# Kernel optimization log

Measured on AMD Instinct MI355X. Metric: run time of the kernel, lower is better.

## Reference

```python
import jax, jax.numpy as jnp
import numpy as np

B, HH, WW, E = 8, 64, 64, 384
NH, EXP = 6, 2
D1 = (EXP * E) // NH * NH      # 768
HD = D1 // NH                  # 128
RPE = 512
LAYERS = 3
EPS = 1e-6


def srms(x):
    # SimpleRMSNorm: no learnable weight
    return x * jax.lax.rsqrt(jnp.mean(x * x, axis=-1, keepdims=True) + EPS)


def rpe_forward(pos, pw, pb, lw, lb, ow, ob):
    # pos: (n, 1) -> (n, NH*HD). Rpe MLP: act(pos_proj) -> layers x [norm,act,linear] -> out
    x = jax.nn.relu(pos @ pw + pb)
    for i in range(lw.shape[0]):  # fixed small layer count
        x = jax.nn.relu(srms(x)) @ lw[i] + lb[i]
    return jax.nn.relu(srms(x)) @ ow + ob


def tno_coeffs(n, pw, pb, lw, lb, ow, ob):
    # Toeplitz coeffs t_0..t_{n-1}, t_0(dummy), t_{-(n-1)}..t_{-1} for circular conv of len 2n
    pos = jnp.arange(1, n, dtype=jnp.float32)[:, None]             # (n-1, 1), par_type=1
    neg = -jnp.arange(1, n, dtype=jnp.float32)[::-1][:, None]      # -(n-1)..-1
    zero = jnp.zeros((1, 1), dtype=jnp.float32)
    t_zero = rpe_forward(zero, pw, pb, lw, lb, ow, ob)             # (1, NH*HD)
    t_pos = rpe_forward(pos, pw, pb, lw, lb, ow, ob)               # (n-1, NH*HD)
    t_neg = rpe_forward(neg, pw, pb, lw, lb, ow, ob)
    a = jnp.concatenate([t_zero, t_pos, t_zero, t_neg], axis=0)    # (2n, NH*HD)
    return a.reshape(2 * n, NH, HD).transpose(1, 0, 2)             # (NH, 2n, HD)


def tno_apply(v, a, axis):
    # v: (b, h, H, W, d); FFT-based Toeplitz (circular) mixing along `axis` in {-3, -2}
    n = v.shape[axis]
    a = a[:, :, None, :] if axis == -3 else a[:, None, :, :]
    y = jnp.fft.rfft(v, 2 * n, axis=axis)
    af = jnp.fft.rfft(a, 2 * n, axis=axis)
    out = jnp.fft.irfft(af * y, 2 * n, axis=axis)
    return jax.lax.slice_in_dim(out, 0, n, axis=out.ndim + axis)


def setup_inputs() -> dict:
    key = jax.random.key(0)
    ks = jax.random.split(key, 24)
    s = 0.02
    def rn(k, shape):
        return jax.random.normal(k, shape, dtype=jnp.float32) * s
    inp = {
        "x": jax.random.normal(ks[0], (B, HH, WW, E), dtype=jnp.float32),
        "H": HH, "W": WW,
        "Wu": rn(ks[1], (E, D1)), "bu": jnp.zeros((D1,), jnp.float32),
        "Wv": rn(ks[2], (E, D1)), "bv": jnp.zeros((D1,), jnp.float32),
        "Wo": rn(ks[3], (D1, E)), "bo": jnp.zeros((E,), jnp.float32),
    }
    for t, off in (("r1", 4), ("r2", 10)):
        inp[t + "_pw"] = rn(ks[off], (1, RPE))
        inp[t + "_pb"] = jnp.zeros((RPE,), jnp.float32)
        inp[t + "_lw"] = rn(ks[off + 1], (LAYERS, RPE, RPE))
        inp[t + "_lb"] = jnp.zeros((LAYERS, RPE), jnp.float32)
        inp[t + "_ow"] = rn(ks[off + 2], (RPE, NH * HD))
        inp[t + "_ob"] = jnp.zeros((NH * HD,), jnp.float32)
    return inp


def reference(x, H, W, Wu, bu, Wv, bv, Wo, bo,
              r1_pw, r1_pb, r1_lw, r1_lb, r1_ow, r1_ob,
              r2_pw, r2_pb, r2_lw, r2_lb, r2_ow, r2_ob):
    b = x.shape[0]
    xn = srms(x)                                    # pre_norm (SimpleRMSNorm)
    u = jax.nn.silu(xn @ Wu + bu)                   # gate branch
    v = jax.nn.silu(xn @ Wv + bv)
    v = v.reshape(b, H, W, NH, HD).transpose(0, 3, 1, 2, 4)        # b h H W d
    a_h = tno_coeffs(H, r2_pw, r2_pb, r2_lw, r2_lb, r2_ow, r2_ob)  # toep2, dim=-3
    a_w = tno_coeffs(W, r1_pw, r1_pb, r1_lw, r1_lb, r1_ow, r1_ob)  # toep1, dim=-2
    out = tno_apply(v, a_h, -3) + tno_apply(v, a_w, -2)
    out = out.transpose(0, 2, 3, 1, 4).reshape(b, H, W, NH * HD)   # b H W (h d)
    out = u * out
    return out @ Wo + bo + x
```

## Files before the change

kernel.cpp:

```cpp
#include <hip/hip_runtime.h>
#include <stdint.h>


typedef __attribute__((ext_vector_type(4))) float  f32x4;
typedef __attribute__((ext_vector_type(8))) short  s16x8;
typedef __attribute__((ext_vector_type(8))) unsigned short u16x8;
typedef __attribute__((ext_vector_type(4))) unsigned short u16x4;
typedef unsigned short u16;

#define M_TOT 32768

__device__ __forceinline__ u16 f2bf(float f) {
  union { float f; unsigned int u; } v; v.f = f;
  unsigned int r = (v.u + 0x7FFFu + ((v.u >> 16) & 1u)) >> 16;
  return (u16)r;
}
__device__ __forceinline__ float bf2f(u16 h) {
  union { unsigned int u; float f; } v; v.u = ((unsigned int)h) << 16;
  return v.f;
}
__device__ __forceinline__ float silu_f(float x) {
  return x * __builtin_amdgcn_rcpf(1.f + __expf(-x));
}

__device__ __forceinline__ void gload_lds16(const u16* g, u16* l) {
  __builtin_amdgcn_global_load_lds(
      (const __attribute__((address_space(1))) uint32_t*)g,
      (__attribute__((address_space(3))) uint32_t*)l, 16, 0, 0);
}

__global__ __launch_bounds__(256) void setup_k(
    const float* __restrict__ x, u16* __restrict__ xn,
    const float* __restrict__ Wu, const float* __restrict__ Wv,
    const float* __restrict__ Wo, u16* __restrict__ Wuvt, u16* __restrict__ Wot,
    const float* __restrict__ r1lw, const float* __restrict__ r1ow,
    const float* __restrict__ r2lw, const float* __restrict__ r2ow,
    u16* __restrict__ lwT, u16* __restrict__ owT,
    const float* __restrict__ r1pw, const float* __restrict__ r1pb,
    const float* __restrict__ r2pw, const float* __restrict__ r2pb,
    float* __restrict__ X0) {
  __shared__ float sm[32][33];
  const int bid = blockIdx.x;
  const int tid = threadIdx.x;

  if (bid < 8192) {
    int row  = bid * 4 + (tid >> 6);
    int lane = tid & 63;
    const float* xr = x + (size_t)row * 384 + lane;
    float v[6]; float ss = 0.f;
#pragma unroll
    for (int i = 0; i < 6; i++) { v[i] = xr[i * 64]; ss += v[i] * v[i]; }
#pragma unroll
    for (int off = 32; off > 0; off >>= 1) ss += __shfl_xor(ss, off);
    float sc = rsqrtf(ss * (1.f / 384.f) + 1e-6f);
    u16* o = xn + (size_t)row * 384 + lane;
#pragma unroll
    for (int i = 0; i < 6; i++) o[i * 64] = f2bf(v[i] * sc);
  } else if (bid < 11360) {
    int b = bid - 8192;
    const float* src; u16* dst; int C, DS, R0, C0;
    if (b < 2304) {
      int mlp = b / 1152, r = b % 1152;
      if (r < 768) {
        int L = r / 256, t = r % 256;
        R0 = (t / 16) * 32; C0 = (t % 16) * 32;
        src = (mlp ? r2lw : r1lw) + (size_t)L * 262144;
        dst = lwT + (size_t)(mlp * 3 + L) * 262144;
        C = 512; DS = 512;
      } else {
        int t = r - 768;
        R0 = (t / 24) * 32; C0 = (t % 24) * 32;
        src = mlp ? r2ow : r1ow;
        dst = owT + (size_t)mlp * 393216;
        C = 768; DS = 512;
      }
    } else {
      int t = b - 2304;
      if (t < 288)      { R0 = (t / 24) * 32; C0 = (t % 24) * 32;
                          src = Wu; C = 768; dst = Wuvt;             DS = 384; }
      else if (t < 576) { int t2 = t - 288; R0 = (t2 / 24) * 32; C0 = (t2 % 24) * 32;
                          src = Wv; C = 768; dst = Wuvt + 768 * 384; DS = 384; }
      else              { int t2 = t - 576; R0 = (t2 / 12) * 32; C0 = (t2 % 12) * 32;
                          src = Wo; C = 384; dst = Wot;              DS = 768; }
    }
    int lx = tid % 32, ly = tid / 32;
#pragma unroll
    for (int q = 0; q < 4; q++) {
      int y = q * 8 + ly;
      sm[y][lx] = src[(size_t)(R0 + y) * C + C0 + lx];
    }
    __syncthreads();
#pragma unroll
    for (int q = 0; q < 4; q++) {
      int y = q * 8 + ly;
      dst[(size_t)(C0 + y) * DS + R0 + lx] = f2bf(sm[lx][y]);
    }
  } else {
    int idx = (bid - 11360) * 256 + tid;
    int gid = idx * 4;
    int row = gid >> 9, col = gid & 511;
    int mlp = row >> 7, p = row & 127;
    float pos = (p < 64) ? (float)p : ((p == 64) ? 0.f : (float)(p - 128));
    const float* pw = (mlp ? r2pw : r1pw) + col;
    const float* pb = (mlp ? r2pb : r1pb) + col;
    f32x4 w = *(const f32x4*)pw;
    f32x4 bb = *(const f32x4*)pb;
    f32x4 o;
#pragma unroll
    for (int e = 0; e < 4; e++) o[e] = fmaxf(pos * w[e] + bb[e], 0.f);
    *(f32x4*)(X0 + gid) = o;
  }
}

template <int N, bool TOUT>
__global__ __launch_bounds__(256) void rpe_layer_k(
    const float* __restrict__ X,
    const u16* __restrict__ wtA, const u16* __restrict__ wtB,
    const float* __restrict__ bA, const float* __restrict__ bB,
    float* __restrict__ outA, float* __restrict__ outB) {
  constexpr int NSL = N / 64;
  const int mlp = blockIdx.x / NSL;
  const int n0  = (blockIdx.x % NSL) * 64;
  const u16* WT = mlp ? wtB : wtA;
  const float* bias = mlp ? bB : bA;
  float* out = mlp ? outB : outA;
  const float* Xm = X + (size_t)mlp * 128 * 512;

  __shared__ __align__(16) u16 Bs[64 * 512];
  __shared__ __align__(16) u16 As[2][128 * 64];
  __shared__ float scale[128];

  const int tid  = threadIdx.x;
  const int lane = tid & 63;
  const int w    = tid >> 6;
  const int fl   = lane & 15, fh = lane >> 4;

#pragma unroll
  for (int r = 0; r < 16; r++) {
    int row  = r * 4 + w;
    int csrc = (lane & ~7) | ((lane & 7) ^ (row & 7));
    gload_lds16(WT + (size_t)(n0 + row) * 512 + csrc * 8,
                Bs + row * 512 + lane * 8);
  }

  {
    int row = tid >> 1, half = tid & 1;
    const float* xr = Xm + (size_t)row * 512 + half * 256;
    float ss = 0.f;
#pragma unroll 8
    for (int q = 0; q < 64; q++) {
      f32x4 v = *(const f32x4*)(xr + q * 4);
      ss += v[0] * v[0] + v[1] * v[1] + v[2] * v[2] + v[3] * v[3];
    }
    ss += __shfl_xor(ss, 1);
    if (!half) scale[row] = rsqrtf(ss * (1.f / 512.f) + 1e-6f);
  }
  __syncthreads();

  int arow[4], akc[4];
  float s_[4];
#pragma unroll
  for (int q = 0; q < 4; q++) {
    int cid = q * 256 + tid;
    arow[q] = cid >> 3;
    akc[q]  = cid & 7;
    s_[q]   = scale[arow[q]];
  }

#pragma unroll
  for (int q = 0; q < 4; q++) {
    const float* xp = Xm + (size_t)arow[q] * 512 + akc[q] * 8;
    f32x4 v0 = *(const f32x4*)xp;
    f32x4 v1 = *(const f32x4*)(xp + 4);
    u16x8 pk;
#pragma unroll
    for (int e = 0; e < 4; e++) pk[e]     = f2bf(fmaxf(v0[e], 0.f) * s_[q]);
#pragma unroll
    for (int e = 0; e < 4; e++) pk[4 + e] = f2bf(fmaxf(v1[e], 0.f) * s_[q]);
    *(u16x8*)(&As[0][arow[q] * 64 + ((akc[q] ^ (arow[q] & 7)) * 8)]) = pk;
  }
  __syncthreads();

  f32x4 acc[2][4];
  {
    f32x4 z = {0.f, 0.f, 0.f, 0.f};
#pragma unroll
    for (int i = 0; i < 2; i++)
#pragma unroll
      for (int j = 0; j < 4; j++) acc[i][j] = z;
  }

  for (int kti = 0; kti < 8; kti++) {
    const int cur = kti & 1;
    f32x4 pf0[4], pf1[4];
    if (kti < 7) {
#pragma unroll
      for (int q = 0; q < 4; q++) {
        const float* xp = Xm + (size_t)arow[q] * 512 + (kti + 1) * 64 + akc[q] * 8;
        pf0[q] = *(const f32x4*)xp;
        pf1[q] = *(const f32x4*)(xp + 4);
      }
    }
#pragma unroll
    for (int ks = 0; ks < 2; ks++) {
      const int xc = ((ks * 4 + fh) ^ (fl & 7)) * 8;
      s16x8 af[2], bfr[4];
#pragma unroll
      for (int i = 0; i < 2; i++)
        af[i] = *(const s16x8*)(&As[cur][(w * 32 + i * 16 + fl) * 64 + xc]);
#pragma unroll
      for (int j = 0; j < 4; j++)
        bfr[j] = *(const s16x8*)(&Bs[(j * 16 + fl) * 512 + kti * 64 + xc]);
#pragma unroll
      for (int i = 0; i < 2; i++)
#pragma unroll
        for (int j = 0; j < 4; j++)
          acc[i][j] = __builtin_amdgcn_mfma_f32_16x16x32_bf16(af[i], bfr[j], acc[i][j], 0, 0, 0);
    }
    if (kti < 7) {
#pragma unroll
      for (int q = 0; q < 4; q++) {
        u16x8 pk;
#pragma unroll
        for (int e = 0; e < 4; e++) pk[e]     = f2bf(fmaxf(pf0[q][e], 0.f) * s_[q]);
#pragma unroll
        for (int e = 0; e < 4; e++) pk[4 + e] = f2bf(fmaxf(pf1[q][e], 0.f) * s_[q]);
        *(u16x8*)(&As[cur ^ 1][arow[q] * 64 + ((akc[q] ^ (arow[q] & 7)) * 8)]) = pk;
      }
    }
    __syncthreads();
  }

#pragma unroll
  for (int i = 0; i < 2; i++)
#pragma unroll
    for (int j = 0; j < 4; j++) {
      int c = n0 + j * 16 + fl;
      float bv_ = bias[c];
#pragma unroll
      for (int q = 0; q < 4; q++) {
        int r = w * 32 + i * 16 + fh * 4 + q;
        if (TOUT) out[(size_t)c * 128 + r] = acc[i][j][q] + bv_;
        else      out[(size_t)r * N + c]   = acc[i][j][q] + bv_;
      }
    }
}

__global__ __launch_bounds__(256) void gemm0_k(
    const u16* __restrict__ A, const u16* __restrict__ Bt,
    u16* __restrict__ u_out, u16* __restrict__ vt_out,
    const float* __restrict__ bu, const float* __restrict__ bv) {
  __shared__ __align__(16) char smem[34816];
  u16*   As  = (u16*)smem;
  u16*   Bs  = As + 128 * 64;
  float* epi = (float*)smem;

  const int tid  = threadIdx.x;
  const int lane = tid & 63;
  const int wid  = tid >> 6;
  const int wm   = wid >> 1, wn = wid & 1;
  const int bm   = blockIdx.x & 255, bn = blockIdx.x >> 8;
  const int m0   = bm * 128, n0 = bn * 128;
  const int fl   = lane & 15, fh = lane >> 4;
  const int K    = 384;

  f32x4 acc[4][4];
  {
    f32x4 z = {0.f, 0.f, 0.f, 0.f};
#pragma unroll
    for (int i = 0; i < 4; i++)
#pragma unroll
      for (int j = 0; j < 4; j++) acc[i][j] = z;
  }

  const int sr  = tid >> 3;
  const int scl = (tid & 7) * 8;
  const int scs = ((tid & 7) ^ (sr & 7)) * 8;

  for (int kt = 0; kt < K; kt += 64) {
    const u16* gA = A  + (size_t)(m0 + sr) * K + kt + scs;
    const u16* gB = Bt + (size_t)(n0 + sr) * K + kt + scs;
    u16* lA = As + sr * 64 + scl;
    u16* lB = Bs + sr * 64 + scl;
#pragma unroll
    for (int i = 0; i < 4; i++) {
      gload_lds16(gA + (size_t)(i * 32) * K, lA + i * 32 * 64);
      gload_lds16(gB + (size_t)(i * 32) * K, lB + i * 32 * 64);
    }
    __syncthreads();
#pragma unroll
    for (int ks = 0; ks < 2; ks++) {
      s16x8 af[4], bfr[4];
      const int xc = ((ks * 4 + fh) ^ (fl & 7)) * 8;
      const u16* ap = As + (wm * 64 + fl) * 64 + xc;
      const u16* bp = Bs + (wn * 64 + fl) * 64 + xc;
#pragma unroll
      for (int i = 0; i < 4; i++) af[i] = *(const s16x8*)(ap + i * 16 * 64);
#pragma unroll
      for (int j = 0; j < 4; j++) bfr[j] = *(const s16x8*)(bp + j * 16 * 64);
#pragma unroll
      for (int i = 0; i < 4; i++)
#pragma unroll
        for (int j = 0; j < 4; j++)
          acc[i][j] = __builtin_amdgcn_mfma_f32_16x16x32_bf16(af[i], bfr[j], acc[i][j], 0, 0, 0);
    }
    __syncthreads();
  }

  for (int half = 0; half < 2; half++) {
    __syncthreads();
    if (wm == half) {
#pragma unroll
      for (int i = 0; i < 4; i++)
#pragma unroll
        for (int j = 0; j < 4; j++) {
          int er = i * 16 + fh * 4;
          int ec = wn * 64 + j * 16 + fl;
#pragma unroll
          for (int q = 0; q < 4; q++) epi[(er + q) * 132 + ec] = acc[i][j][q];
        }
    }
    __syncthreads();
    const bool isU = (n0 < 768);
    u16* baseo = isU ? u_out : vt_out;
    const int cc = tid >> 1;
    const int cg = (isU ? n0 : n0 - 768) + cc;
    const float bias_v = (isU ? bu : bv)[cg];
    u16* dst = baseo + (size_t)cg * M_TOT + m0 + half * 64;
#pragma unroll
    for (int q = 0; q < 4; q++) {
      int mb = (tid & 1) * 8 + q * 16;
      u16x8 pk;
#pragma unroll
      for (int e = 0; e < 8; e++) {
        int mm = mb + e;
        pk[e] = f2bf(silu_f(epi[mm * 132 + cc] + bias_v));
      }
      *(u16x8*)(dst + mb) = pk;
    }
  }
}

__global__ __launch_bounds__(512, 2) void gemm2_k(
    const u16* __restrict__ gT, const u16* __restrict__ Wot,
    float* __restrict__ out, const float* __restrict__ bo,
    const float* __restrict__ xres) {
  __shared__ __align__(16) u16 As[128 * 64];
  __shared__ __align__(16) u16 Bs[384 * 64];

  const int tid  = threadIdx.x;
  const int lane = tid & 63;
  const int wid  = tid >> 6;
  const int wm   = wid >> 2;
  const int wn   = wid & 3;
  const int m0   = blockIdx.x * 128;
  const int fl   = lane & 15, fh = lane >> 4;

  f32x4 acc[4][6];
  {
    f32x4 z = {0.f, 0.f, 0.f, 0.f};
#pragma unroll
    for (int i = 0; i < 4; i++)
#pragma unroll
      for (int j = 0; j < 6; j++) acc[i][j] = z;
  }

  const int sr  = tid >> 3;
  const int scl = (tid & 7) * 8;
  const int scs = ((tid & 7) ^ (sr & 7)) * 8;

  for (int kt = 0; kt < 768; kt += 64) {
#pragma unroll
    for (int i = 0; i < 6; i++)
      gload_lds16(Wot + (size_t)(sr + 64 * i) * 768 + kt + scs,
                  Bs + (sr + 64 * i) * 64 + scl);
#pragma unroll
    for (int r = 0; r < 2; r++) {
      int cid = r * 512 + tid;
      int row = cid >> 4;
      int cm  = cid & 15;
      const u16* ga = gT + (size_t)(kt + row) * M_TOT + m0 + cm * 8;
      u16x8 rv = *(const u16x8*)ga;
      int kc = row >> 3, of = row & 7;
#pragma unroll
      for (int e = 0; e < 8; e++)
        As[(cm * 8 + e) * 64 + ((kc ^ e) << 3) + of] = rv[e];
    }
    __syncthreads();
#pragma unroll
    for (int ks = 0; ks < 2; ks++) {
      s16x8 af[4], bfr[6];
      const int xc = ((ks * 4 + fh) ^ (fl & 7)) * 8;
      const u16* ap = As + (wm * 64 + fl) * 64 + xc;
      const u16* bp = Bs + (wn * 96 + fl) * 64 + xc;
#pragma unroll
      for (int i = 0; i < 4; i++) af[i] = *(const s16x8*)(ap + i * 16 * 64);
#pragma unroll
      for (int j = 0; j < 6; j++) bfr[j] = *(const s16x8*)(bp + j * 16 * 64);
#pragma unroll
      for (int i = 0; i < 4; i++)
#pragma unroll
        for (int j = 0; j < 6; j++)
          acc[i][j] = __builtin_amdgcn_mfma_f32_16x16x32_bf16(af[i], bfr[j], acc[i][j], 0, 0, 0);
    }
    __syncthreads();
  }

  float bov[6];
#pragma unroll
  for (int j = 0; j < 6; j++) bov[j] = bo[wn * 96 + j * 16 + fl];
#pragma unroll
  for (int i = 0; i < 4; i++) {
#pragma unroll
    for (int q = 0; q < 4; q++) {
      int m = m0 + wm * 64 + i * 16 + fh * 4 + q;
      const float* xr = xres + (size_t)m * 384;
      float* orow = out + (size_t)m * 384;
#pragma unroll
      for (int j = 0; j < 6; j++) {
        int n = wn * 96 + j * 16 + fl;
        orow[n] = acc[i][j][q] + bov[j] + xr[n];
      }
    }
  }
}

__global__ __launch_bounds__(256) void conv_k(const u16* __restrict__ vt,
                                              const u16* __restrict__ ut,
                                              const float* __restrict__ a_hT,
                                              const float* __restrict__ a_wT,
                                              u16* __restrict__ gT) {
  __shared__ __align__(16) u16 Th[64 * 72];
  __shared__ __align__(16) u16 Tw[64 * 72];
  __shared__ __align__(16) u16 Vs[64 * 72];
  __shared__ __align__(16) u16 VTs[64 * 72];
  __shared__ __align__(16) u16 Us[64 * 72];
  __shared__ float ahr[192];
  __shared__ float awr[192];
  u16* epi = VTs;

  const int tid = threadIdx.x;
  const int c = blockIdx.x;
  const int lane = tid & 63, w = tid >> 6;
  const int fl = lane & 15, fh = lane >> 4;

  if (tid < 192) {
    int idx = (128 - tid) & 127;
    ahr[tid] = a_hT[(size_t)c * 128 + idx];
    awr[tid] = a_wT[(size_t)c * 128 + idx];
  }
  __syncthreads();

  {
    int y = tid & 63, j0 = (tid >> 6) * 16;
    int base = 128 - y + j0;
    u16x8 p0, p1, q0, q1;
#pragma unroll
    for (int e = 0; e < 8; e++) {
      p0[e] = f2bf(ahr[base + e]);
      p1[e] = f2bf(ahr[base + 8 + e]);
      q0[e] = f2bf(awr[base + e]);
      q1[e] = f2bf(awr[base + 8 + e]);
    }
    *(u16x8*)(Th + y * 72 + j0)     = p0;
    *(u16x8*)(Th + y * 72 + j0 + 8) = p1;
    *(u16x8*)(Tw + y * 72 + j0)     = q0;
    *(u16x8*)(Tw + y * 72 + j0 + 8) = q1;
  }

  const int sy = tid >> 2, sx = (tid & 3) * 16;
  const int ty = tid & 63, tj = (tid >> 6) * 16;

  for (int b = 0; b < 8; b++) {
    const u16* srcv = vt + (size_t)c * M_TOT + b * 4096;
    const u16* srcu = ut + (size_t)c * M_TOT + b * 4096;
    *(u16x8*)(Vs + sy * 72 + sx)     = *(const u16x8*)(srcv + sy * 64 + sx);
    *(u16x8*)(Vs + sy * 72 + sx + 8) = *(const u16x8*)(srcv + sy * 64 + sx + 8);
    *(u16x8*)(Us + sy * 72 + sx)     = *(const u16x8*)(srcu + sy * 64 + sx);
    *(u16x8*)(Us + sy * 72 + sx + 8) = *(const u16x8*)(srcu + sy * 64 + sx + 8);
    __syncthreads();

    {
      u16x8 q0 = *(const u16x8*)(Vs + ty * 72 + tj);
      u16x8 q1 = *(const u16x8*)(Vs + ty * 72 + tj + 8);
#pragma unroll
      for (int e = 0; e < 8; e++) VTs[(tj + e) * 72 + ty]     = q0[e];
#pragma unroll
      for (int e = 0; e < 8; e++) VTs[(tj + 8 + e) * 72 + ty] = q1[e];
    }
    __syncthreads();

    f32x4 acc[4];
    {
      f32x4 z = {0.f, 0.f, 0.f, 0.f};
#pragma unroll
      for (int i = 0; i < 4; i++) acc[i] = z;
    }
#pragma unroll
    for (int ks = 0; ks < 2; ks++) {
      s16x8 qh = *(const s16x8*)(Th + (w * 16 + fl) * 72 + ks * 32 + fh * 8);
#pragma unroll
      for (int i = 0; i < 4; i++) {
        s16x8 p = *(const s16x8*)(VTs + (i * 16 + fl) * 72 + ks * 32 + fh * 8);
        acc[i] = __builtin_amdgcn_mfma_f32_16x16x32_bf16(p, qh, acc[i], 0, 0, 0);
      }
      s16x8 qw = *(const s16x8*)(Vs + (w * 16 + fl) * 72 + ks * 32 + fh * 8);
#pragma unroll
      for (int i = 0; i < 4; i++) {
        s16x8 p = *(const s16x8*)(Tw + (i * 16 + fl) * 72 + ks * 32 + fh * 8);
        acc[i] = __builtin_amdgcn_mfma_f32_16x16x32_bf16(p, qw, acc[i], 0, 0, 0);
      }
    }
    __syncthreads();

    {
      int y = w * 16 + fl;
#pragma unroll
      for (int i = 0; i < 4; i++) {
        u16x4 uq = *(const u16x4*)(Us + y * 72 + i * 16 + fh * 4);
        u16x4 pk;
#pragma unroll
        for (int e = 0; e < 4; e++) pk[e] = f2bf(acc[i][e] * bf2f(uq[e]));
        *(u16x4*)(epi + y * 72 + i * 16 + fh * 4) = pk;
      }
    }
    __syncthreads();

    {
      u16x8 a0 = *(const u16x8*)(epi + sy * 72 + sx);
      u16x8 a1 = *(const u16x8*)(epi + sy * 72 + sx + 8);
      u16* dst = gT + (size_t)c * M_TOT + b * 4096 + sy * 64 + sx;
      *(u16x8*)dst = a0;
      *(u16x8*)(dst + 8) = a1;
    }
    __syncthreads();
  }
}

extern "C" void kernel_launch(void* const* d_in, const int* in_sizes, int n_in,
                              void* d_out, int out_size, void* d_ws, size_t ws_size,
                              hipStream_t stream) {
  const float* x    = (const float*)d_in[0];
  const float* Wu   = (const float*)d_in[3];
  const float* bu   = (const float*)d_in[4];
  const float* Wv   = (const float*)d_in[5];
  const float* bv   = (const float*)d_in[6];
  const float* Wo   = (const float*)d_in[7];
  const float* bo   = (const float*)d_in[8];
  const float* r1pw = (const float*)d_in[9];
  const float* r1pb = (const float*)d_in[10];
  const float* r1lw = (const float*)d_in[11];
  const float* r1lb = (const float*)d_in[12];
  const float* r1ow = (const float*)d_in[13];
  const float* r1ob = (const float*)d_in[14];
  const float* r2pw = (const float*)d_in[15];
  const float* r2pb = (const float*)d_in[16];
  const float* r2lw = (const float*)d_in[17];
  const float* r2lb = (const float*)d_in[18];
  const float* r2ow = (const float*)d_in[19];
  const float* r2ob = (const float*)d_in[20];
  float* outp = (float*)d_out;

  char* ws = (char*)d_ws;
  size_t off = 0;
  auto carve = [&](size_t bytes) {
    char* p = ws + off;
    off += (bytes + 255) & ~(size_t)255;
    return p;
  };
  u16*   xn   = (u16*)carve((size_t)M_TOT * 384 * 2);
  u16*   uT   = (u16*)carve((size_t)768 * M_TOT * 2);
  u16*   vT   = (u16*)carve((size_t)768 * M_TOT * 2);
  u16*   gT   = (u16*)carve((size_t)768 * M_TOT * 2);
  u16*   Wuvt = (u16*)carve((size_t)1536 * 384 * 2);
  u16*   Wot  = (u16*)carve((size_t)384 * 768 * 2);
  float* awT  = (float*)carve((size_t)768 * 128 * 4);
  float* ahT  = (float*)carve((size_t)768 * 128 * 4);

  char* rb  = (char*)gT;
  u16*   lwT = (u16*)rb;
  u16*   owT = (u16*)(rb + 3145728);
  float* X0  = (float*)(rb + 3145728 + 1572864);
  float* X1  = X0 + 256 * 512;

  setup_k<<<11488, 256, 0, stream>>>(x, xn, Wu, Wv, Wo, Wuvt, Wot,
                                     r1lw, r1ow, r2lw, r2ow, lwT, owT,
                                     r1pw, r1pb, r2pw, r2pb, X0);

  rpe_layer_k<512, false><<<16, 256, 0, stream>>>(X0, lwT, lwT + 3 * 262144,
                                                  r1lb, r2lb, X1, X1 + 128 * 512);
  rpe_layer_k<512, false><<<16, 256, 0, stream>>>(X1, lwT + 262144, lwT + 4 * 262144,
                                                  r1lb + 512, r2lb + 512, X0, X0 + 128 * 512);
  rpe_layer_k<512, false><<<16, 256, 0, stream>>>(X0, lwT + 2 * 262144, lwT + 5 * 262144,
                                                  r1lb + 1024, r2lb + 1024, X1, X1 + 128 * 512);
  rpe_layer_k<768, true><<<24, 256, 0, stream>>>(X1, owT, owT + 393216,
                                                 r1ob, r2ob, awT, ahT);

  gemm0_k<<<256 * 12, 256, 0, stream>>>(xn, Wuvt, uT, vT, bu, bv);
  conv_k<<<768, 256, 0, stream>>>(vT, uT, ahT, awT, gT);
  gemm2_k<<<256, 512, 0, stream>>>(gT, Wot, outp, bo, x);
}
```

Baseline: 366.3 us.

## Enlarge gemm0 tile to 128x256 and prefetch global loads in gemm2 and conv

gemm0 now uses 512 threads per block with a 128x256 output tile, so each A tile is loaded once for twice as many columns, halving the grid. Its epilogue goes through LDS in four quarters with a stride-133 layout to cut bank conflicts. gemm2 and conv_k now register-prefetch the next K-slice or batch slice of global data while computing on the current one, hiding load latency. conv_k also drops its trailing barrier, which relies on the existing barriers to protect LDS reuse, and the changes add register pressure.

```diff
diff --git a/kernel.cpp b/kernel.cpp
--- a/kernel.cpp
+++ b/kernel.cpp
@@ -246,11 +246,11 @@
     }
 }
 
-__global__ __launch_bounds__(256) void gemm0_k(
+__global__ __launch_bounds__(512) void gemm0_k(
     const u16* __restrict__ A, const u16* __restrict__ Bt,
     u16* __restrict__ u_out, u16* __restrict__ vt_out,
     const float* __restrict__ bu, const float* __restrict__ bv) {
-  __shared__ __align__(16) char smem[34816];
+  __shared__ __align__(16) char smem[49152];
   u16*   As  = (u16*)smem;
   u16*   Bs  = As + 128 * 64;
   float* epi = (float*)smem;
@@ -258,9 +258,10 @@
   const int tid  = threadIdx.x;
   const int lane = tid & 63;
   const int wid  = tid >> 6;
-  const int wm   = wid >> 1, wn = wid & 1;
+  const int wm   = wid >> 2;
+  const int wn   = wid & 3;
   const int bm   = blockIdx.x & 255, bn = blockIdx.x >> 8;
-  const int m0   = bm * 128, n0 = bn * 128;
+  const int m0   = bm * 128, n0 = bn * 256;
   const int fl   = lane & 15, fh = lane >> 4;
   const int K    = 384;
 
@@ -273,20 +274,17 @@
       for (int j = 0; j < 4; j++) acc[i][j] = z;
   }
 
-  const int sr  = tid >> 3;
-  const int scl = (tid & 7) * 8;
-  const int scs = ((tid & 7) ^ (sr & 7)) * 8;
+  const int ra = tid >> 3;
+  const int ca = tid & 7;
+  const int swc = (ca ^ (ra & 7)) * 8;
 
   for (int kt = 0; kt < K; kt += 64) {
-    const u16* gA = A  + (size_t)(m0 + sr) * K + kt + scs;
-    const u16* gB = Bt + (size_t)(n0 + sr) * K + kt + scs;
-    u16* lA = As + sr * 64 + scl;
-    u16* lB = Bs + sr * 64 + scl;
-#pragma unroll
-    for (int i = 0; i < 4; i++) {
-      gload_lds16(gA + (size_t)(i * 32) * K, lA + i * 32 * 64);
-      gload_lds16(gB + (size_t)(i * 32) * K, lB + i * 32 * 64);
-    }
+    gload_lds16(A + (size_t)(m0 + ra) * K + kt + swc,        As + ra * 64 + ca * 8);
+    gload_lds16(A + (size_t)(m0 + 64 + ra) * K + kt + swc,   As + (64 + ra) * 64 + ca * 8);
+#pragma unroll
+    for (int q = 0; q < 4; q++)
+      gload_lds16(Bt + (size_t)(n0 + q * 64 + ra) * K + kt + swc,
+                  Bs + (q * 64 + ra) * 64 + ca * 8);
     __syncthreads();
 #pragma unroll
     for (int ks = 0; ks < 2; ks++) {
@@ -307,36 +305,39 @@
     __syncthreads();
   }
 
-  for (int half = 0; half < 2; half++) {
-    __syncthreads();
-    if (wm == half) {
-#pragma unroll
-      for (int i = 0; i < 4; i++)
-#pragma unroll
-        for (int j = 0; j < 4; j++) {
-          int er = i * 16 + fh * 4;
-          int ec = wn * 64 + j * 16 + fl;
-#pragma unroll
-          for (int q = 0; q < 4; q++) epi[(er + q) * 132 + ec] = acc[i][j][q];
-        }
-    }
-    __syncthreads();
-    const bool isU = (n0 < 768);
-    u16* baseo = isU ? u_out : vt_out;
-    const int cc = tid >> 1;
-    const int cg = (isU ? n0 : n0 - 768) + cc;
-    const float bias_v = (isU ? bu : bv)[cg];
-    u16* dst = baseo + (size_t)cg * M_TOT + m0 + half * 64;
-#pragma unroll
-    for (int q = 0; q < 4; q++) {
-      int mb = (tid & 1) * 8 + q * 16;
-      u16x8 pk;
+#pragma unroll
+  for (int mh = 0; mh < 2; mh++) {
+#pragma unroll
+    for (int nh = 0; nh < 2; nh++) {
+      __syncthreads();
+      if (wm == mh && (wn >> 1) == nh) {
+        int nq = wn & 1;
+#pragma unroll
+        for (int i = 0; i < 4; i++)
+#pragma unroll
+          for (int j = 0; j < 4; j++) {
+            int er = i * 16 + fh * 4;
+            int ec = nq * 64 + j * 16 + fl;
+#pragma unroll
+            for (int q = 0; q < 4; q++) epi[(er + q) * 133 + ec] = acc[i][j][q];
+          }
+      }
+      __syncthreads();
+      int cc = tid >> 2;
+      int cg = n0 + nh * 128 + cc;
+      const bool isU = (cg < 768);
+      const int cgm = isU ? cg : cg - 768;
+      const float bias_v = (isU ? bu : bv)[cgm];
+      u16* dst = (isU ? u_out : vt_out) + (size_t)cgm * M_TOT + m0 + mh * 64 + (tid & 3) * 16;
+      u16x8 pk0, pk1;
+      const int mb = (tid & 3) * 16;
 #pragma unroll
       for (int e = 0; e < 8; e++) {
-        int mm = mb + e;
-        pk[e] = f2bf(silu_f(epi[mm * 132 + cc] + bias_v));
-      }
-      *(u16x8*)(dst + mb) = pk;
+        pk0[e] = f2bf(silu_f(epi[(mb + e) * 133 + cc] + bias_v));
+        pk1[e] = f2bf(silu_f(epi[(mb + 8 + e) * 133 + cc] + bias_v));
+      }
+      *(u16x8*)dst = pk0;
+      *(u16x8*)(dst + 8) = pk1;
     }
   }
 }
@@ -369,6 +370,19 @@
   const int scl = (tid & 7) * 8;
   const int scs = ((tid & 7) ^ (sr & 7)) * 8;
 
+  int arw[2], acm[2];
+#pragma unroll
+  for (int r = 0; r < 2; r++) {
+    int cid = r * 512 + tid;
+    arw[r] = cid >> 4;
+    acm[r] = cid & 15;
+  }
+
+  u16x8 rv[2];
+#pragma unroll
+  for (int r = 0; r < 2; r++)
+    rv[r] = *(const u16x8*)(gT + (size_t)arw[r] * M_TOT + m0 + acm[r] * 8);
+
   for (int kt = 0; kt < 768; kt += 64) {
 #pragma unroll
     for (int i = 0; i < 6; i++)
@@ -376,17 +390,17 @@
                   Bs + (sr + 64 * i) * 64 + scl);
 #pragma unroll
     for (int r = 0; r < 2; r++) {
-      int cid = r * 512 + tid;
-      int row = cid >> 4;
-      int cm  = cid & 15;
-      const u16* ga = gT + (size_t)(kt + row) * M_TOT + m0 + cm * 8;
-      u16x8 rv = *(const u16x8*)ga;
-      int kc = row >> 3, of = row & 7;
+      int kc = arw[r] >> 3, of = arw[r] & 7;
 #pragma unroll
       for (int e = 0; e < 8; e++)
-        As[(cm * 8 + e) * 64 + ((kc ^ e) << 3) + of] = rv[e];
-    }
-    __syncthreads();
+        As[(acm[r] * 8 + e) * 64 + ((kc ^ e) << 3) + of] = rv[r][e];
+    }
+    __syncthreads();
+    if (kt < 704) {
+#pragma unroll
+      for (int r = 0; r < 2; r++)
+        rv[r] = *(const u16x8*)(gT + (size_t)(kt + 64 + arw[r]) * M_TOT + m0 + acm[r] * 8);
+    }
 #pragma unroll
     for (int ks = 0; ks < 2; ks++) {
       s16x8 af[4], bfr[6];
@@ -471,14 +485,29 @@
   const int sy = tid >> 2, sx = (tid & 3) * 16;
   const int ty = tid & 63, tj = (tid >> 6) * 16;
 
+  const u16* srcv0 = vt + (size_t)c * M_TOT;
+  const u16* srcu0 = ut + (size_t)c * M_TOT;
+
+  u16x8 pv0 = *(const u16x8*)(srcv0 + sy * 64 + sx);
+  u16x8 pv1 = *(const u16x8*)(srcv0 + sy * 64 + sx + 8);
+  u16x8 pu0 = *(const u16x8*)(srcu0 + sy * 64 + sx);
+  u16x8 pu1 = *(const u16x8*)(srcu0 + sy * 64 + sx + 8);
+
   for (int b = 0; b < 8; b++) {
-    const u16* srcv = vt + (size_t)c * M_TOT + b * 4096;
-    const u16* srcu = ut + (size_t)c * M_TOT + b * 4096;
-    *(u16x8*)(Vs + sy * 72 + sx)     = *(const u16x8*)(srcv + sy * 64 + sx);
-    *(u16x8*)(Vs + sy * 72 + sx + 8) = *(const u16x8*)(srcv + sy * 64 + sx + 8);
-    *(u16x8*)(Us + sy * 72 + sx)     = *(const u16x8*)(srcu + sy * 64 + sx);
-    *(u16x8*)(Us + sy * 72 + sx + 8) = *(const u16x8*)(srcu + sy * 64 + sx + 8);
-    __syncthreads();
+    *(u16x8*)(Vs + sy * 72 + sx)     = pv0;
+    *(u16x8*)(Vs + sy * 72 + sx + 8) = pv1;
+    *(u16x8*)(Us + sy * 72 + sx)     = pu0;
+    *(u16x8*)(Us + sy * 72 + sx + 8) = pu1;
+    __syncthreads();
+
+    if (b < 7) {
+      const u16* nv = srcv0 + (b + 1) * 4096 + sy * 64 + sx;
+      const u16* nu = srcu0 + (b + 1) * 4096 + sy * 64 + sx;
+      pv0 = *(const u16x8*)nv;
+      pv1 = *(const u16x8*)(nv + 8);
+      pu0 = *(const u16x8*)nu;
+      pu1 = *(const u16x8*)(nu + 8);
+    }
 
     {
       u16x8 q0 = *(const u16x8*)(Vs + ty * 72 + tj);
@@ -533,7 +562,6 @@
       *(u16x8*)dst = a0;
       *(u16x8*)(dst + 8) = a1;
     }
-    __syncthreads();
   }
 }
 
@@ -596,7 +624,7 @@
   rpe_layer_k<768, true><<<24, 256, 0, stream>>>(X1, owT, owT + 393216,
                                                  r1ob, r2ob, awT, ahT);
 
-  gemm0_k<<<256 * 12, 256, 0, stream>>>(xn, Wuvt, uT, vT, bu, bv);
+  gemm0_k<<<256 * 6, 512, 0, stream>>>(xn, Wuvt, uT, vT, bu, bv);
   conv_k<<<768, 256, 0, stream>>>(vT, uT, ahT, awT, gT);
   gemm2_k<<<256, 512, 0, stream>>>(gT, Wot, outp, bo, x);
 }
```

After: 384.6 us. 5.0% more time.
